# Performance work log

Measured on AMD Instinct MI355X. Metric: run time of the kernel, lower is better.

The kernel has to match this reference:

```python
import jax, jax.numpy as jnp
import numpy as np

B, SQ, SKV = 4, 4096, 1024
QDIM, CDIM = 1024, 768
HEADS, DHEAD = 16, 64
INNER = HEADS * DHEAD


def setup_inputs() -> dict:
    key = jax.random.key(0)
    ks = jax.random.split(key, 7)
    s = 0.02
    return {
        "x": jax.random.normal(ks[0], (B, SQ, QDIM), dtype=jnp.float32),
        "context": jax.random.normal(ks[1], (B, SKV, CDIM), dtype=jnp.float32),
        "Wq": jax.random.normal(ks[2], (QDIM, INNER), dtype=jnp.float32) * s,
        "Wk": jax.random.normal(ks[3], (CDIM, INNER), dtype=jnp.float32) * s,
        "Wv": jax.random.normal(ks[4], (CDIM, INNER), dtype=jnp.float32) * s,
        "Wo": jax.random.normal(ks[5], (INNER, QDIM), dtype=jnp.float32) * s,
        "bo": jnp.zeros((QDIM,), dtype=jnp.float32),
    }


def reference(x, context, Wq, Wk, Wv, Wo, bo):
    # QKV projections (no bias, matching bias=False Linear layers)
    q = x @ Wq          # [B, SQ, INNER]
    k = context @ Wk    # [B, SKV, INNER]
    v = context @ Wv    # [B, SKV, INNER]

    # split heads: b s (h d) -> b h s d
    def split_heads(t, s):
        return t.reshape(B, s, HEADS, DHEAD).transpose(0, 2, 1, 3)

    qh = split_heads(q, SQ)
    kh = split_heads(k, SKV)
    vh = split_heads(v, SKV)

    scale = DHEAD ** -0.5  # attention_basic default scale
    sim = jnp.einsum('bhqd,bhkd->bhqk', qh, kh) * scale  # [B,H,SQ,SKV]
    attn = jax.nn.softmax(sim, axis=-1)
    out = jnp.einsum('bhqk,bhkd->bhqd', attn, vh)        # [B,H,SQ,DHEAD]
    out = out.transpose(0, 2, 1, 3).reshape(B, SQ, INNER)

    # output projection (Linear with bias); dropout p=0 -> identity
    return out @ Wo + bo
```

## Files before the change

### kernel.cpp

```cpp
#include <hip/hip_runtime.h>


typedef unsigned short u16;
typedef unsigned int u32;
typedef __bf16 bf16x8 __attribute__((ext_vector_type(8)));
typedef float float4v __attribute__((ext_vector_type(4)));
typedef _Float16 half4 __attribute__((ext_vector_type(4)));
typedef _Float16 half2v __attribute__((ext_vector_type(2)));
typedef __attribute__((address_space(1))) void as1_void;
typedef __attribute__((address_space(3))) void as3_void;

__device__ __forceinline__ u16 f2bf(float f) {
  unsigned u = __float_as_uint(f);
  u += 0x7FFF + ((u >> 16) & 1);
  return (u16)(u >> 16);
}

__device__ __forceinline__ void async16(const u16* g, u16* l) {
  __builtin_amdgcn_global_load_lds((as1_void*)(void*)g, (as3_void*)l, 16, 0, 0);
}

#define WAITCNT_VM8 0xF78
#define WAITCNT_VM4 0xF74
#define WAITCNT_VM0 0xF70

__global__ void cvt_kernel(const float* __restrict__ x, u16* __restrict__ xbf,
                           const float* __restrict__ ctx, u16* __restrict__ ctxbf) {
  int i = blockIdx.x * 256 + threadIdx.x;
  const float* in; u16* out; int j;
  if (i < 4194304) { in = x; out = xbf; j = i; }
  else if (i < 4980736) { in = ctx; out = ctxbf; j = i - 4194304; }
  else return;
  float4 v = ((const float4*)in)[j];
  ushort4 o;
  o.x = f2bf(v.x); o.y = f2bf(v.y); o.z = f2bf(v.z); o.w = f2bf(v.w);
  ((ushort4*)out)[j] = o;
}

__global__ void twt_kernel(const float* __restrict__ Wq, const float* __restrict__ Wk,
                           const float* __restrict__ Wv, const float* __restrict__ Wo,
                           u16* __restrict__ WqT, u16* __restrict__ WkT,
                           u16* __restrict__ WvT, u16* __restrict__ WoT) {
  __shared__ u16 t[32][33];
  int z = blockIdx.z;
  const float* W = z == 0 ? Wq : z == 1 ? Wk : z == 2 ? Wv : Wo;
  u16* Wt = z == 0 ? WqT : z == 1 ? WkT : z == 2 ? WvT : WoT;
  int Kd = (z == 1 || z == 2) ? 768 : 1024;
  int k0 = blockIdx.y * 32;
  if (k0 >= Kd) return;
  int tx = threadIdx.x, ty = threadIdx.y;
  int n0 = blockIdx.x * 32;
#pragma unroll
  for (int i = 0; i < 4; i++)
    t[ty + i * 8][tx] = f2bf(W[(size_t)(k0 + ty + i * 8) * 1024 + n0 + tx]);
  __syncthreads();
#pragma unroll
  for (int i = 0; i < 4; i++)
    Wt[(size_t)(n0 + ty + i * 8) * Kd + k0 + tx] = t[tx][ty + i * 8];
}

__device__ __forceinline__ void gemm128_core(const u16* __restrict__ A,
                                             const u16* __restrict__ Bt, int K,
                                             int m0, int n0, float4v acc[4][4]) {
  __shared__ __align__(16) u16 L[3][2][128][32];
  int tid = threadIdx.x;
  int w = tid >> 6, lane = tid & 63;
  int l15 = lane & 15, quad = lane >> 4;
  int wm = (w >> 1) * 64, wn = (w & 1) * 64;

  const u16* pA = A + (size_t)(m0 + (tid >> 2)) * K + (tid & 3) * 8;
  const u16* pB = Bt + (size_t)(n0 + (tid >> 2)) * K + (tid & 3) * 8;
  size_t r64 = (size_t)64 * K;
  int dofs = tid * 8;

#define STG(buf, t)                                                            \
  do {                                                                         \
    const u16* sa = pA + (size_t)(t) * 32;                                     \
    const u16* sb = pB + (size_t)(t) * 32;                                     \
    async16(sa, &L[buf][0][0][0] + dofs);                                      \
    async16(sa + r64, &L[buf][0][0][0] + dofs + 2048);                         \
    async16(sb, &L[buf][1][0][0] + dofs);                                      \
    async16(sb + r64, &L[buf][1][0][0] + dofs + 2048);                         \
  } while (0)

  STG(0, 0);
  STG(1, 1);

  int niter = K >> 5;
  int cb = 0;
  for (int it = 0; it < niter; ++it) {
    if (it + 1 < niter) __builtin_amdgcn_s_waitcnt(WAITCNT_VM4);
    else                __builtin_amdgcn_s_waitcnt(WAITCNT_VM0);
    __builtin_amdgcn_s_barrier();
    if (it + 2 < niter) {
      int pb = cb + 2; if (pb >= 3) pb -= 3;
      STG(pb, it + 2);
    }
    const u16* cA = &L[cb][0][0][0];
    const u16* cB = &L[cb][1][0][0];
    bf16x8 fa[4], fb[4];
#pragma unroll
    for (int mi = 0; mi < 4; mi++)
      fa[mi] = *(const bf16x8*)&cA[(wm + mi * 16 + l15) * 32 + quad * 8];
#pragma unroll
    for (int ni = 0; ni < 4; ni++)
      fb[ni] = *(const bf16x8*)&cB[(wn + ni * 16 + l15) * 32 + quad * 8];
    __builtin_amdgcn_s_setprio(1);
#pragma unroll
    for (int mi = 0; mi < 4; mi++)
#pragma unroll
      for (int ni = 0; ni < 4; ni++)
        acc[mi][ni] = __builtin_amdgcn_mfma_f32_16x16x32_bf16(fa[mi], fb[ni], acc[mi][ni], 0, 0, 0);
    __builtin_amdgcn_s_setprio(0);
    cb = (cb + 1 == 3) ? 0 : cb + 1;
  }
#undef STG
}

__global__ __launch_bounds__(256, 3) void qkv_gemm128(
    const u16* __restrict__ xbf, const u16* __restrict__ ctxbf,
    const u16* __restrict__ WqT, const u16* __restrict__ WkT, const u16* __restrict__ WvT,
    u16* __restrict__ Qb, u16* __restrict__ Kbuf, u16* __restrict__ Vtb, float qscale) {
  int bx0 = blockIdx.x;
  int bx = (bx0 & 7) * 192 + (bx0 >> 3);
  const u16* A; const u16* Bt; u16* C; int K, mode, m0, n0; float scale;
  if (bx < 1024)      { int t = bx;        A = xbf;   Bt = WqT; C = Qb;   K = 1024; mode = 0; scale = qscale; m0 = (t >> 3) * 128; n0 = (t & 7) * 128; }
  else if (bx < 1280) { int t = bx - 1024; A = ctxbf; Bt = WkT; C = Kbuf; K = 768;  mode = 0; scale = 1.0f;   m0 = (t >> 3) * 128; n0 = (t & 7) * 128; }
  else                { int t = bx - 1280; A = ctxbf; Bt = WvT; C = Vtb;  K = 768;  mode = 2; scale = 1.0f;   m0 = (t >> 3) * 128; n0 = (t & 7) * 128; }

  float4v acc[4][4] = {};
  gemm128_core(A, Bt, K, m0, n0, acc);

  int tid = threadIdx.x;
  int w = tid >> 6, lane = tid & 63;
  int l15 = lane & 15, quad = lane >> 4;
  int wm = (w >> 1) * 64, wn = (w & 1) * 64;

  if (mode == 0) {
#pragma unroll
    for (int mi = 0; mi < 4; mi++) {
      int rowb = m0 + wm + mi * 16 + quad * 4;
#pragma unroll
      for (int ni = 0; ni < 4; ni++) {
        int col = n0 + wn + ni * 16 + l15;
#pragma unroll
        for (int r = 0; r < 4; r++)
          C[(size_t)(rowb + r) * 1024 + col] = f2bf(acc[mi][ni][r] * scale);
      }
    }
  } else {
#pragma unroll
    for (int mi = 0; mi < 4; mi++) {
      int rowb = m0 + wm + mi * 16 + quad * 4;
#pragma unroll
      for (int ni = 0; ni < 4; ni++) {
        int col = n0 + wn + ni * 16 + l15;
        int hh = col >> 6, dd = col & 63;
#pragma unroll
        for (int r = 0; r < 4; r++) {
          int rr = rowb + r;
          int b = rr >> 10, skv = rr & 1023;
          _Float16 hv = (_Float16)acc[mi][ni][r];
          C[((((size_t)b * 16 + hh) * 64 + dd) << 10) + skv] = __builtin_bit_cast(u16, hv);
        }
      }
    }
  }
}

__global__ __launch_bounds__(256, 3) void gemm_bt128(
    const u16* __restrict__ A, const u16* __restrict__ Bt,
    float* __restrict__ C, const float* __restrict__ bias) {
  int bx0 = blockIdx.x;
  int bx = (bx0 & 7) * 128 + (bx0 >> 3);
  int m0 = (bx >> 3) * 128, n0 = (bx & 7) * 128;

  float4v acc[4][4] = {};
  gemm128_core(A, Bt, 1024, m0, n0, acc);

  int tid = threadIdx.x;
  int w = tid >> 6, lane = tid & 63;
  int l15 = lane & 15, quad = lane >> 4;
  int wm = (w >> 1) * 64, wn = (w & 1) * 64;

#pragma unroll
  for (int mi = 0; mi < 4; mi++) {
    int rowb = m0 + wm + mi * 16 + quad * 4;
#pragma unroll
    for (int ni = 0; ni < 4; ni++) {
      int col = n0 + wn + ni * 16 + l15;
      float bv = bias[col];
#pragma unroll
      for (int r = 0; r < 4; r++)
        C[(size_t)(rowb + r) * 1024 + col] = acc[mi][ni][r] + bv;
    }
  }
}

__global__ __launch_bounds__(512, 4) void attn_kernel(
    const u16* __restrict__ Q, const u16* __restrict__ Kb,
    const u16* __restrict__ Vt, u16* __restrict__ Oout) {
  __shared__ __align__(16) u16 lK[2][8192];
  __shared__ __align__(16) u16 lV[2][8192];
  int tid = threadIdx.x, w = tid >> 6, lane = tid & 63;
  int l15 = lane & 15, quad = lane >> 4;
  int bh = blockIdx.y, b = bh >> 4, h = bh & 15;
  int q0 = blockIdx.x * 256 + w * 32;

  const u16* Qbase = Q + ((size_t)(b * 4096 + q0)) * 1024 + h * 64;
  const u16* Kbase = Kb + ((size_t)b << 20) + h * 64;
  const u16* Vbase = Vt + ((size_t)bh << 16);

  bf16x8 qf[2][2];
#pragma unroll
  for (int qt = 0; qt < 2; qt++)
#pragma unroll
    for (int c = 0; c < 2; c++)
      qf[qt][c] = *(const bf16x8*)(Qbase + (size_t)(qt * 16 + l15) * 1024 + c * 32 + quad * 8);

  int kr0 = tid >> 3, kx0 = ((tid & 7) ^ (kr0 & 7)) * 8;
  const u16* ks0 = Kbase + (size_t)kr0 * 1024 + kx0;
  const u16* ks1 = ks0 + (size_t)64 * 1024;
  int vd0 = tid >> 4, vc0 = ((tid & 15) ^ (vd0 & 15)) * 8;
  const u16* vs0 = Vbase + (size_t)vd0 * 1024 + vc0;
  const u16* vs1 = vs0 + (size_t)32 * 1024;
  int kdo0 = w * 512, kdo1 = 4096 + w * 512;

  async16(ks0, &lK[0][kdo0]); async16(ks1, &lK[0][kdo1]);
  async16(vs0, &lV[0][kdo0]); async16(vs1, &lV[0][kdo1]);
  ks0 += 131072; ks1 += 131072;
  vs0 += 128; vs1 += 128;

  float4v o[2][4] = {};
  float4v osum[2] = {};
  const half4 ones = {(_Float16)1.0f, (_Float16)1.0f, (_Float16)1.0f, (_Float16)1.0f};

  int lb = l15 & 7;
  int xk0 = ((0 + quad) ^ lb) * 16 + l15 * 128;
  int xk1 = ((4 + quad) ^ lb) * 16 + l15 * 128;
  int qh = quad >> 1, qo = (quad & 1) * 8;
  int vrow = l15 * 256 + qo;

  for (int it = 0; it < 8; ++it) {
    const char* bK = (const char*)lK + (it & 1) * 16384;
    const char* bV = (const char*)lV + (it & 1) * 16384;
    __syncthreads();
    if (it < 7) {
      int nb = (it + 1) & 1;
      async16(ks0, &lK[nb][kdo0]); async16(ks1, &lK[nb][kdo1]);
      async16(vs0, &lV[nb][kdo0]); async16(vs1, &lV[nb][kdo1]);
      ks0 += 131072; ks1 += 131072;
      vs0 += 128; vs1 += 128;
    }
#pragma unroll
    for (int ss = 0; ss < 8; ss++) {
      int sub = (ss + w) & 7;
      int sb = sub * 2048;
      float4v sv[2] = {{0.f, 0.f, 0.f, 0.f}, {0.f, 0.f, 0.f, 0.f}};
      __builtin_amdgcn_s_setprio(1);
#pragma unroll
      for (int c = 0; c < 2; c++) {
        bf16x8 kf = *(const bf16x8*)(bK + sb + (c ? xk1 : xk0));
#pragma unroll
        for (int qt = 0; qt < 2; qt++)
          sv[qt] = __builtin_amdgcn_mfma_f32_16x16x32_bf16(kf, qf[qt][c], sv[qt], 0, 0, 0);
      }
      __builtin_amdgcn_s_setprio(0);
      half4 pf[2];
#pragma unroll
      for (int qt = 0; qt < 2; qt++) {
        float e0 = exp2f(sv[qt][0]), e1 = exp2f(sv[qt][1]);
        float e2 = exp2f(sv[qt][2]), e3 = exp2f(sv[qt][3]);
        half2v p01 = __builtin_bit_cast(half2v, __builtin_amdgcn_cvt_pkrtz(e0, e1));
        half2v p23 = __builtin_bit_cast(half2v, __builtin_amdgcn_cvt_pkrtz(e2, e3));
        pf[qt] = __builtin_shufflevector(p01, p23, 0, 1, 2, 3);
        osum[qt] = __builtin_amdgcn_mfma_f32_16x16x16f16(ones, pf[qt], osum[qt], 0, 0, 0);
      }
      int vbs = vrow + (((sub * 2 + qh) ^ l15) * 16);
      __builtin_amdgcn_s_setprio(1);
#pragma unroll
      for (int dt = 0; dt < 4; dt++) {
        half4 vf = *(const half4*)(bV + dt * 4096 + vbs);
#pragma unroll
        for (int qt = 0; qt < 2; qt++)
          o[qt][dt] = __builtin_amdgcn_mfma_f32_16x16x16f16(vf, pf[qt], o[qt][dt], 0, 0, 0);
      }
      __builtin_amdgcn_s_setprio(0);
    }
  }

#pragma unroll
  for (int qt = 0; qt < 2; qt++) {
    float inv = 1.0f / osum[qt][0];
    u16* Ob = Oout + ((size_t)(b * 4096 + q0 + qt * 16 + l15)) * 1024 + h * 64 + quad * 4;
#pragma unroll
    for (int dt = 0; dt < 4; dt++) {
      ushort4 pk;
      pk.x = f2bf(o[qt][dt][0] * inv);
      pk.y = f2bf(o[qt][dt][1] * inv);
      pk.z = f2bf(o[qt][dt][2] * inv);
      pk.w = f2bf(o[qt][dt][3] * inv);
      *(ushort4*)(Ob + dt * 16) = pk;
    }
  }
}

extern "C" void kernel_launch(void* const* d_in, const int* in_sizes, int n_in,
                              void* d_out, int out_size, void* d_ws, size_t ws_size,
                              hipStream_t stream) {
  const float* x   = (const float*)d_in[0];
  const float* ctx = (const float*)d_in[1];
  const float* Wq  = (const float*)d_in[2];
  const float* Wk  = (const float*)d_in[3];
  const float* Wv  = (const float*)d_in[4];
  const float* Wo  = (const float*)d_in[5];
  const float* bo  = (const float*)d_in[6];
  float* out = (float*)d_out;

  u16* ws    = (u16*)d_ws;
  u16* xbf   = ws;
  u16* ctxbf = xbf + 16777216;
  u16* WqT   = ctxbf + 3145728;
  u16* WkT   = WqT + 1048576;
  u16* WvT   = WkT + 786432;
  u16* WoT   = WvT + 786432;
  u16* Qb    = WoT + 1048576;
  u16* Kbuf  = Qb + 16777216;
  u16* Vtb   = Kbuf + 4194304;
  if (ws_size < (size_t)48758784 * 2) return;

  cvt_kernel<<<19456, 256, 0, stream>>>(x, xbf, ctx, ctxbf);
  twt_kernel<<<dim3(32, 32, 4), dim3(32, 8), 0, stream>>>(Wq, Wk, Wv, Wo, WqT, WkT, WvT, WoT);
  qkv_gemm128<<<dim3(1536), dim3(256), 0, stream>>>(xbf, ctxbf, WqT, WkT, WvT,
                                                    Qb, Kbuf, Vtb, 0.18033688011112042f);
  attn_kernel<<<dim3(16, 64), dim3(512), 0, stream>>>(Qb, Kbuf, Vtb, xbf);
  gemm_bt128<<<dim3(1024), dim3(256), 0, stream>>>(xbf, WoT, out, bo);
}
```

Before: 346.9 us.

## Use 256x128 GEMM tiles with 8 waves, swizzled LDS, and fused prep kernel

Both projection GEMMs move from 128x128 tiles with 4 waves to 256x128 tiles with 8 waves. Each B tile is now shared by twice as many output rows, which is meant to cut global traffic per FLOP. The LDS pipeline drops from triple to double buffering with a full vmcnt(0) wait each iteration, and adds an XOR swizzle on the 16-byte chunks to reduce bank conflicts. The activation conversion and weight transpose kernels are merged into a single launch to save one kernel launch. The trade-off is less latency hiding from the shallower pipeline, and fewer, larger blocks that may reduce occupancy or balance across CUs.

```diff
diff --git a/kernel.cpp b/kernel.cpp
--- a/kernel.cpp
+++ b/kernel.cpp
@@ -20,36 +20,39 @@
   __builtin_amdgcn_global_load_lds((as1_void*)(void*)g, (as3_void*)l, 16, 0, 0);
 }
 
-#define WAITCNT_VM8 0xF78
-#define WAITCNT_VM4 0xF74
 #define WAITCNT_VM0 0xF70
 
-__global__ void cvt_kernel(const float* __restrict__ x, u16* __restrict__ xbf,
-                           const float* __restrict__ ctx, u16* __restrict__ ctxbf) {
-  int i = blockIdx.x * 256 + threadIdx.x;
-  const float* in; u16* out; int j;
-  if (i < 4194304) { in = x; out = xbf; j = i; }
-  else if (i < 4980736) { in = ctx; out = ctxbf; j = i - 4194304; }
-  else return;
-  float4 v = ((const float4*)in)[j];
-  ushort4 o;
-  o.x = f2bf(v.x); o.y = f2bf(v.y); o.z = f2bf(v.z); o.w = f2bf(v.w);
-  ((ushort4*)out)[j] = o;
-}
-
-__global__ void twt_kernel(const float* __restrict__ Wq, const float* __restrict__ Wk,
-                           const float* __restrict__ Wv, const float* __restrict__ Wo,
-                           u16* __restrict__ WqT, u16* __restrict__ WkT,
-                           u16* __restrict__ WvT, u16* __restrict__ WoT) {
+__global__ void prep_kernel(const float* __restrict__ x, u16* __restrict__ xbf,
+                            const float* __restrict__ ctx, u16* __restrict__ ctxbf,
+                            const float* __restrict__ Wq, const float* __restrict__ Wk,
+                            const float* __restrict__ Wv, const float* __restrict__ Wo,
+                            u16* __restrict__ WqT, u16* __restrict__ WkT,
+                            u16* __restrict__ WvT, u16* __restrict__ WoT) {
   __shared__ u16 t[32][33];
-  int z = blockIdx.z;
+  int blk = blockIdx.x;
+  if (blk < 19456) {
+    int i = blk * 256 + threadIdx.x;
+    const float* in; u16* out; int j;
+    if (i < 4194304) { in = x; out = xbf; j = i; }
+    else if (i < 4980736) { in = ctx; out = ctxbf; j = i - 4194304; }
+    else return;
+    float4 v = ((const float4*)in)[j];
+    ushort4 o;
+    o.x = f2bf(v.x); o.y = f2bf(v.y); o.z = f2bf(v.z); o.w = f2bf(v.w);
+    ((ushort4*)out)[j] = o;
+    return;
+  }
+  int rem = blk - 19456;
+  int z = rem >> 10, r1 = rem & 1023;
+  int by = r1 >> 5, bxx = r1 & 31;
   const float* W = z == 0 ? Wq : z == 1 ? Wk : z == 2 ? Wv : Wo;
   u16* Wt = z == 0 ? WqT : z == 1 ? WkT : z == 2 ? WvT : WoT;
   int Kd = (z == 1 || z == 2) ? 768 : 1024;
-  int k0 = blockIdx.y * 32;
+  int k0 = by * 32;
   if (k0 >= Kd) return;
-  int tx = threadIdx.x, ty = threadIdx.y;
-  int n0 = blockIdx.x * 32;
+  int tid = threadIdx.x;
+  int tx = tid & 31, ty = tid >> 5;
+  int n0 = bxx * 32;
 #pragma unroll
   for (int i = 0; i < 4; i++)
     t[ty + i * 8][tx] = f2bf(W[(size_t)(k0 + ty + i * 8) * 1024 + n0 + tx]);
@@ -59,52 +62,45 @@
     Wt[(size_t)(n0 + ty + i * 8) * Kd + k0 + tx] = t[tx][ty + i * 8];
 }
 
-__device__ __forceinline__ void gemm128_core(const u16* __restrict__ A,
-                                             const u16* __restrict__ Bt, int K,
-                                             int m0, int n0, float4v acc[4][4]) {
-  __shared__ __align__(16) u16 L[3][2][128][32];
+__device__ __forceinline__ void gemm_h_core(const u16* __restrict__ A,
+                                            const u16* __restrict__ Bt, int K,
+                                            int m0, int n0, float4v acc[4][4]) {
+  __shared__ __align__(16) u16 L[2][12288];
   int tid = threadIdx.x;
   int w = tid >> 6, lane = tid & 63;
   int l15 = lane & 15, quad = lane >> 4;
   int wm = (w >> 1) * 64, wn = (w & 1) * 64;
 
-  const u16* pA = A + (size_t)(m0 + (tid >> 2)) * K + (tid & 3) * 8;
-  const u16* pB = Bt + (size_t)(n0 + (tid >> 2)) * K + (tid & 3) * 8;
-  size_t r64 = (size_t)64 * K;
+  int r0 = tid >> 2, s0 = tid & 3;
+  int gx = (s0 ^ (r0 & 3)) << 3;
+  const u16* pA0 = A + (size_t)(m0 + r0) * K + gx;
+  const u16* pA1 = pA0 + (size_t)128 * K;
+  const u16* pB  = Bt + (size_t)(n0 + r0) * K + gx;
   int dofs = tid * 8;
 
 #define STG(buf, t)                                                            \
   do {                                                                         \
-    const u16* sa = pA + (size_t)(t) * 32;                                     \
-    const u16* sb = pB + (size_t)(t) * 32;                                     \
-    async16(sa, &L[buf][0][0][0] + dofs);                                      \
-    async16(sa + r64, &L[buf][0][0][0] + dofs + 2048);                         \
-    async16(sb, &L[buf][1][0][0] + dofs);                                      \
-    async16(sb + r64, &L[buf][1][0][0] + dofs + 2048);                         \
+    async16(pA0 + (size_t)(t) * 32, &L[buf][dofs]);                            \
+    async16(pA1 + (size_t)(t) * 32, &L[buf][4096 + dofs]);                     \
+    async16(pB + (size_t)(t) * 32, &L[buf][8192 + dofs]);                      \
   } while (0)
 
   STG(0, 0);
-  STG(1, 1);
-
   int niter = K >> 5;
-  int cb = 0;
+  int cur = 0;
+  int lb2 = l15 & 3;
   for (int it = 0; it < niter; ++it) {
-    if (it + 1 < niter) __builtin_amdgcn_s_waitcnt(WAITCNT_VM4);
-    else                __builtin_amdgcn_s_waitcnt(WAITCNT_VM0);
+    __builtin_amdgcn_s_waitcnt(WAITCNT_VM0);
     __builtin_amdgcn_s_barrier();
-    if (it + 2 < niter) {
-      int pb = cb + 2; if (pb >= 3) pb -= 3;
-      STG(pb, it + 2);
-    }
-    const u16* cA = &L[cb][0][0][0];
-    const u16* cB = &L[cb][1][0][0];
+    if (it + 1 < niter) STG(cur ^ 1, it + 1);
+    const u16* Lb = &L[cur][0];
     bf16x8 fa[4], fb[4];
 #pragma unroll
     for (int mi = 0; mi < 4; mi++)
-      fa[mi] = *(const bf16x8*)&cA[(wm + mi * 16 + l15) * 32 + quad * 8];
+      fa[mi] = *(const bf16x8*)&Lb[(wm + mi * 16 + l15) * 32 + ((quad ^ lb2) << 3)];
 #pragma unroll
     for (int ni = 0; ni < 4; ni++)
-      fb[ni] = *(const bf16x8*)&cB[(wn + ni * 16 + l15) * 32 + quad * 8];
+      fb[ni] = *(const bf16x8*)&Lb[8192 + (wn + ni * 16 + l15) * 32 + ((quad ^ lb2) << 3)];
     __builtin_amdgcn_s_setprio(1);
 #pragma unroll
     for (int mi = 0; mi < 4; mi++)
@@ -112,24 +108,24 @@
       for (int ni = 0; ni < 4; ni++)
         acc[mi][ni] = __builtin_amdgcn_mfma_f32_16x16x32_bf16(fa[mi], fb[ni], acc[mi][ni], 0, 0, 0);
     __builtin_amdgcn_s_setprio(0);
-    cb = (cb + 1 == 3) ? 0 : cb + 1;
+    cur ^= 1;
   }
 #undef STG
 }
 
-__global__ __launch_bounds__(256, 3) void qkv_gemm128(
+__global__ __launch_bounds__(512, 4) void qkv_gemm_h(
     const u16* __restrict__ xbf, const u16* __restrict__ ctxbf,
     const u16* __restrict__ WqT, const u16* __restrict__ WkT, const u16* __restrict__ WvT,
     u16* __restrict__ Qb, u16* __restrict__ Kbuf, u16* __restrict__ Vtb, float qscale) {
   int bx0 = blockIdx.x;
-  int bx = (bx0 & 7) * 192 + (bx0 >> 3);
+  int bx = (bx0 & 7) * 96 + (bx0 >> 3);
   const u16* A; const u16* Bt; u16* C; int K, mode, m0, n0; float scale;
-  if (bx < 1024)      { int t = bx;        A = xbf;   Bt = WqT; C = Qb;   K = 1024; mode = 0; scale = qscale; m0 = (t >> 3) * 128; n0 = (t & 7) * 128; }
-  else if (bx < 1280) { int t = bx - 1024; A = ctxbf; Bt = WkT; C = Kbuf; K = 768;  mode = 0; scale = 1.0f;   m0 = (t >> 3) * 128; n0 = (t & 7) * 128; }
-  else                { int t = bx - 1280; A = ctxbf; Bt = WvT; C = Vtb;  K = 768;  mode = 2; scale = 1.0f;   m0 = (t >> 3) * 128; n0 = (t & 7) * 128; }
+  if (bx < 512)      { int t = bx;       A = xbf;   Bt = WqT; C = Qb;   K = 1024; mode = 0; scale = qscale; m0 = (t >> 3) * 256; n0 = (t & 7) * 128; }
+  else if (bx < 640) { int t = bx - 512; A = ctxbf; Bt = WkT; C = Kbuf; K = 768;  mode = 0; scale = 1.0f;   m0 = (t >> 3) * 256; n0 = (t & 7) * 128; }
+  else               { int t = bx - 640; A = ctxbf; Bt = WvT; C = Vtb;  K = 768;  mode = 2; scale = 1.0f;   m0 = (t >> 3) * 256; n0 = (t & 7) * 128; }
 
   float4v acc[4][4] = {};
-  gemm128_core(A, Bt, K, m0, n0, acc);
+  gemm_h_core(A, Bt, K, m0, n0, acc);
 
   int tid = threadIdx.x;
   int w = tid >> 6, lane = tid & 63;
@@ -168,15 +164,15 @@
   }
 }
 
-__global__ __launch_bounds__(256, 3) void gemm_bt128(
+__global__ __launch_bounds__(512, 4) void gemm_bt_h(
     const u16* __restrict__ A, const u16* __restrict__ Bt,
     float* __restrict__ C, const float* __restrict__ bias) {
   int bx0 = blockIdx.x;
-  int bx = (bx0 & 7) * 128 + (bx0 >> 3);
-  int m0 = (bx >> 3) * 128, n0 = (bx & 7) * 128;
+  int bx = (bx0 & 7) * 64 + (bx0 >> 3);
+  int m0 = (bx >> 3) * 256, n0 = (bx & 7) * 128;
 
   float4v acc[4][4] = {};
-  gemm128_core(A, Bt, 1024, m0, n0, acc);
+  gemm_h_core(A, Bt, 1024, m0, n0, acc);
 
   int tid = threadIdx.x;
   int w = tid >> 6, lane = tid & 63;
@@ -329,10 +325,10 @@
   u16* Vtb   = Kbuf + 4194304;
   if (ws_size < (size_t)48758784 * 2) return;
 
-  cvt_kernel<<<19456, 256, 0, stream>>>(x, xbf, ctx, ctxbf);
-  twt_kernel<<<dim3(32, 32, 4), dim3(32, 8), 0, stream>>>(Wq, Wk, Wv, Wo, WqT, WkT, WvT, WoT);
-  qkv_gemm128<<<dim3(1536), dim3(256), 0, stream>>>(xbf, ctxbf, WqT, WkT, WvT,
-                                                    Qb, Kbuf, Vtb, 0.18033688011112042f);
+  prep_kernel<<<23552, 256, 0, stream>>>(x, xbf, ctx, ctxbf,
+                                         Wq, Wk, Wv, Wo, WqT, WkT, WvT, WoT);
+  qkv_gemm_h<<<dim3(768), dim3(512), 0, stream>>>(xbf, ctxbf, WqT, WkT, WvT,
+                                                  Qb, Kbuf, Vtb, 0.18033688011112042f);
   attn_kernel<<<dim3(16, 64), dim3(512), 0, stream>>>(Qb, Kbuf, Vtb, xbf);
-  gemm_bt128<<<dim3(1024), dim3(256), 0, stream>>>(xbf, WoT, out, bo);
-}
+  gemm_bt_h<<<dim3(512), dim3(512), 0, stream>>>(xbf, WoT, out, bo);
+}
```

New measurement: 343.7 us. No clear change (-0.9%).
